# Optimization experiments

Measured on AMD Instinct MI355X. Metric: run time of the kernel, lower is better.

The kernel has to match this reference:

```python
import jax, jax.numpy as jnp
import numpy as np

L = 5   # local window size (l)
R = 2   # upsample factor (r)


def setup_inputs() -> dict:
    key = jax.random.key(0)
    k0, k1, k2 = jax.random.split(key, 3)
    B, C, H, W, OUT = 4, 128, 64, 64, 128
    x = jax.random.normal(k0, (B, C, H, W), jnp.float32)
    # conv1: in_channels -> l^2, 3x3, pad 1 (with bias, as nn.Conv2d default)
    w1 = jax.random.normal(k1, (L * L, C, 3, 3), jnp.float32) * 0.05
    b1 = jnp.zeros((L * L,), jnp.float32)
    # conv2: 4*in_channels -> out_channels, 1x1 (stored as [out, 4C])
    w2 = jax.random.normal(k2, (OUT, 4 * C), jnp.float32) * 0.05
    b2 = jnp.zeros((OUT,), jnp.float32)
    return {"x": x, "w1": w1, "b1": b1, "w2": w2, "b2": b2}


def _upsample2_nearest(t):
    # nearest-neighbor x2 upsample on NCHW
    return jnp.repeat(jnp.repeat(t, R, axis=2), R, axis=3)


def reference(x, w1, b1, w2, b2):
    B, C, H, W = x.shape
    # conv1 (3x3, SAME) -> [B, L^2, H, W]
    k = jax.lax.conv_general_dilated(
        x, w1, window_strides=(1, 1), padding='SAME',
        dimension_numbers=('NCHW', 'OIHW', 'NCHW')) + b1[None, :, None, None]
    # nearest x2 upsample then softmax over the L^2 channel dim
    k = _upsample2_nearest(k)                 # [B, L^2, 2H, 2W]
    k = jax.nn.softmax(k, axis=1)
    # non-overlapping RxR block extraction (unfold size=R, step=R twice)
    # -> [B, L^2, H, W, R^2], last-dim order (row-offset, col-offset)
    k = k.reshape(B, L * L, H, R, W, R).transpose(0, 1, 2, 4, 3, 5)
    k = k.reshape(B, L * L, H, W, R * R)
    # overlapping LxL window extraction of the input (unfold size=L, step=1)
    pad = L // 2
    xp = jnp.pad(x, ((0, 0), (0, 0), (pad, pad), (pad, pad)))
    wins = jnp.stack(
        [xp[:, :, i:i + H, j:j + W] for i in range(L) for j in range(L)],
        axis=-1)                               # [B, C, H, W, L^2]
    # per-pixel matmul: [C, L^2] @ [L^2, R^2] -> [B, H, W, C, R^2]
    out = jnp.einsum('bchwk,bkhwr->bhwcr', wins, k)
    # flatten (C, R^2) -> 4C (C-major, matching torch reshape), back to NCHW
    out = out.reshape(B, H, W, C * R * R).transpose(0, 3, 1, 2)
    out = _upsample2_nearest(out)              # [B, 4C, 2H, 2W]
    # conv2: 1x1 -> out_channels
    out = jnp.einsum('bchw,oc->bohw', out, w2) + b2[None, :, None, None]
    return out
```

## Files before the change

### kernel.cpp

```cpp
#include <hip/hip_runtime.h>
#include <math.h>

#define BB   4
#define CC   128
#define HH   64
#define WW   64
#define OUTC 128
#define KK   25
#define PXB  16
#define SJ   20

typedef __attribute__((ext_vector_type(8))) short short8;
typedef __attribute__((ext_vector_type(4))) float floatx4;

__device__ __forceinline__ unsigned short f32_to_bf16(float v) {
    unsigned int u = __float_as_uint(v);
    u += 0x7fffu + ((u >> 16) & 1u);
    return (unsigned short)(u >> 16);
}
__device__ __forceinline__ float bf16_to_f32(unsigned short h) {
    return __uint_as_float(((unsigned int)h) << 16);
}

__global__ void prep_kernel(const float* __restrict__ w2,
                            const float* __restrict__ w1,
                            unsigned short* __restrict__ w2o,
                            unsigned short* __restrict__ w1f) {
    int i = blockIdx.x * 256 + threadIdx.x;
    if (i < 16384) {
        int o = i >> 7, c = i & 127;
        const float* p = w2 + o * (4 * CC) + c * 4;
        w2o[o * CC + c] = f32_to_bf16(p[0] + p[1] + p[2] + p[3]);
    } else {
        int f = i - 16384;
        int i8 = f & 7;  int rest = f >> 3;
        int lane = rest & 63; rest >>= 6;
        int ks = rest & 3;  rest >>= 2;
        int mt = rest & 1;  rest >>= 1;
        int dydx = rest % 9;
        int wt   = rest / 9;
        int kk = mt * 16 + (lane & 15);
        int c  = ks * 32 + (lane >> 4) * 8 + i8;
        unsigned short o16 = 0;
        if (kk < KK) {
            float v = w1[(size_t)(kk * CC + c) * 9 + dydx];
            unsigned short hi = f32_to_bf16(v);
            o16 = wt ? f32_to_bf16(v - bf16_to_f32(hi)) : hi;
        }
        w1f[f] = o16;
    }
}

__global__ __launch_bounds__(128, 2) void fused_kernel(
        const float* __restrict__ x,
        const unsigned short* __restrict__ w1f,
        const unsigned short* __restrict__ w2o,
        const float* __restrict__ b1,
        const float* __restrict__ b2,
        float* __restrict__ out) {
    __shared__ unsigned short xs_hi[3 * SJ * 128];
    __shared__ unsigned short xs_lo[3 * SJ * 128];
    __shared__ float pk[KK * PXB];
    __shared__ float blds[32];
    unsigned short* sKT = xs_hi;

    int bid0 = blockIdx.x;
    int bid  = (bid0 & 7) * 128 + (bid0 >> 3);
    int wq = bid & 3;
    int h  = (bid >> 2) & 63;
    int b  = bid >> 8;
    int t  = threadIdx.x;
    int lane = t & 63;
    int wv = t >> 6;

    const float* xb = x + (size_t)b * CC * (HH * WW);

    if (t < KK) blds[t] = b1[t];
    {
        int jj = lane & 15, cc = lane >> 4;
        int j  = jj + 2;
        int swz = (j & 15) << 3;
        for (int ci = 0; ci < 16; ++ci) {
            int c  = wv * 64 + ci * 4 + cc;
            int cs = c ^ swz;
            const float* xc = xb + (size_t)c * (HH * WW) + wq * 16 + jj;
            #pragma unroll
            for (int r = 0; r < 3; ++r) {
                int y = h - 1 + r;
                float v = (y >= 0 && y < HH) ? xc[y * WW] : 0.f;
                unsigned short hi = f32_to_bf16(v);
                unsigned short lo = f32_to_bf16(v - bf16_to_f32(hi));
                xs_hi[(r * SJ + j) * 128 + cs] = hi;
                xs_lo[(r * SJ + j) * 128 + cs] = lo;
            }
        }
        for (int i = t; i < 3 * 4 * 128; i += 128) {
            int jh = i & 3;
            int c  = (i >> 2) & 127;
            int r  = i >> 9;
            int j2 = (jh < 2) ? jh : 16 + jh;
            int xcol = wq * 16 + j2 - 2;
            int y = h - 1 + r;
            float v = (xcol >= 0 && xcol < WW && y >= 0 && y < HH)
                    ? xb[(size_t)c * (HH * WW) + y * WW + xcol] : 0.f;
            unsigned short hi = f32_to_bf16(v);
            unsigned short lo = f32_to_bf16(v - bf16_to_f32(hi));
            int cs2 = c ^ ((j2 & 15) << 3);
            xs_hi[(r * SJ + j2) * 128 + cs2] = hi;
            xs_lo[(r * SJ + j2) * 128 + cs2] = lo;
        }
    }
    __syncthreads();

    int fpx = lane & 15, quad = lane >> 4;
    int mt = wv;
    floatx4 acc = {0.f, 0.f, 0.f, 0.f};
    for (int dydx = 0; dydx < 9; ++dydx) {
        int r   = dydx / 3;
        int dxm = dydx - 3 * r;
        int j   = fpx + dxm + 1;
        int rowbase = (r * SJ + j) * 128;
        int swz = (j & 15) << 3;
        const unsigned short* whb = w1f + (dydx * 2 + mt) * 2048 + lane * 8;
        #pragma unroll
        for (int ks = 0; ks < 4; ++ks) {
            int cb = (ks * 32 + quad * 8) ^ swz;
            short8 Ah = *(const short8*)(whb + ks * 512);
            short8 Al = *(const short8*)(whb + 36864 + ks * 512);
            short8 Bh = *(const short8*)&xs_hi[rowbase + cb];
            short8 Bl = *(const short8*)&xs_lo[rowbase + cb];
            acc = __builtin_amdgcn_mfma_f32_16x16x32_bf16(Ah, Bh, acc, 0, 0, 0);
            acc = __builtin_amdgcn_mfma_f32_16x16x32_bf16(Ah, Bl, acc, 0, 0, 0);
            acc = __builtin_amdgcn_mfma_f32_16x16x32_bf16(Al, Bh, acc, 0, 0, 0);
        }
    }
    #pragma unroll
    for (int reg = 0; reg < 4; ++reg) {
        int kk = mt * 16 + quad * 4 + reg;
        if (kk < KK) pk[kk * PXB + fpx] = acc[reg] + blds[kk];
    }
    __syncthreads();

    int pp2 = t & 7, cw = t >> 3;

    float2 lg[KK];
    #pragma unroll
    for (int k = 0; k < KK; ++k) lg[k] = *(const float2*)&pk[k * PXB + 2 * pp2];
    float m0 = -1e30f, m1 = -1e30f;
    #pragma unroll
    for (int k = 0; k < KK; ++k) { m0 = fmaxf(m0, lg[k].x); m1 = fmaxf(m1, lg[k].y); }
    float s0 = 0.f, s1 = 0.f;
    #pragma unroll
    for (int k = 0; k < KK; ++k) {
        lg[k].x = __expf(lg[k].x - m0); s0 += lg[k].x;
        lg[k].y = __expf(lg[k].y - m1); s1 += lg[k].y;
    }
    float i0 = 1.f / s0, i1 = 1.f / s1;
    #pragma unroll
    for (int k = 0; k < KK; ++k) { lg[k].x *= i0; lg[k].y *= i1; }

    int colg = wq * 16 + 2 * pp2 - 2;
    int coff[3]; float cmask[3];
    #pragma unroll
    for (int jx = 0; jx < 3; ++jx) {
        int cg = colg + 2 * jx;
        cmask[jx] = (cg >= 0 && cg <= WW - 2) ? 1.f : 0.f;
        coff[jx]  = min(max(cg, 0), WW - 2);
    }
    int yoff[5]; float msk[15];
    #pragma unroll
    for (int di = 0; di < 5; ++di) {
        int y = h + di - 2;
        float rm = (y >= 0 && y < HH) ? 1.f : 0.f;
        yoff[di] = min(max(y, 0), HH - 1) * WW;
        #pragma unroll
        for (int jx = 0; jx < 3; ++jx) msk[di * 3 + jx] = rm * cmask[jx];
    }

    #pragma unroll 2
    for (int i8 = 0; i8 < 8; ++i8) {
        int c = i8 * 16 + cw;
        const float* xc = xb + (size_t)c * (HH * WW);
        float2 xv[15];
        #pragma unroll
        for (int di = 0; di < 5; ++di)
            #pragma unroll
            for (int jx = 0; jx < 3; ++jx) {
                float2 v = *(const float2*)(xc + yoff[di] + coff[jx]);
                float mm = msk[di * 3 + jx];
                xv[di * 3 + jx] = make_float2(v.x * mm, v.y * mm);
            }
        float t0 = 0.f, t1 = 0.f;
        #pragma unroll
        for (int di = 0; di < 5; ++di) {
            float2 x01 = xv[di * 3 + 0];
            float2 x23 = xv[di * 3 + 1];
            float2 x45 = xv[di * 3 + 2];
            t0 += lg[di*5+0].x * x01.x + lg[di*5+1].x * x01.y
                + lg[di*5+2].x * x23.x + lg[di*5+3].x * x23.y
                + lg[di*5+4].x * x45.x;
            t1 += lg[di*5+0].y * x01.y + lg[di*5+1].y * x23.x
                + lg[di*5+2].y * x23.y + lg[di*5+3].y * x45.x
                + lg[di*5+4].y * x45.y;
        }
        sKT[(2 * pp2) * 136 + c]     = f32_to_bf16(t0);
        sKT[(2 * pp2 + 1) * 136 + c] = f32_to_bf16(t1);
    }
    __syncthreads();

    floatx4 am[4] = {{0.f,0.f,0.f,0.f},{0.f,0.f,0.f,0.f},
                     {0.f,0.f,0.f,0.f},{0.f,0.f,0.f,0.f}};
    #pragma unroll
    for (int ks = 0; ks < 4; ++ks) {
        short8 bf = *(const short8*)&sKT[fpx * 136 + ks*32 + quad*8];
        #pragma unroll
        for (int mt2 = 0; mt2 < 4; ++mt2) {
            short8 af = *(const short8*)&w2o[(size_t)(64*wv + 16*mt2 + fpx) * CC
                                             + ks*32 + quad*8];
            am[mt2] = __builtin_amdgcn_mfma_f32_16x16x32_bf16(af, bf, am[mt2], 0, 0, 0);
        }
    }

    float* ob = out + (size_t)b * OUTC * (4 * HH * WW);
    int y0 = 2 * h;
    int pxo = wq * 16 + fpx;
    #pragma unroll
    for (int mt2 = 0; mt2 < 4; ++mt2) {
        #pragma unroll
        for (int reg = 0; reg < 4; ++reg) {
            int o = 64*wv + 16*mt2 + quad*4 + reg;
            float v = am[mt2][reg] + b2[o];
            float2 v2 = make_float2(v, v);
            float* r0p = ob + ((size_t)o * (2*HH) + y0) * (2*WW) + 2*pxo;
            *(float2*)(r0p)        = v2;
            *(float2*)(r0p + 2*WW) = v2;
        }
    }
}

extern "C" void kernel_launch(void* const* d_in, const int* in_sizes, int n_in,
                              void* d_out, int out_size, void* d_ws, size_t ws_size,
                              hipStream_t stream) {
    const float* x  = (const float*)d_in[0];
    const float* w1 = (const float*)d_in[1];
    const float* b1 = (const float*)d_in[2];
    const float* w2 = (const float*)d_in[3];
    const float* b2 = (const float*)d_in[4];
    float* out = (float*)d_out;

    unsigned short* w2o = (unsigned short*)d_ws;
    unsigned short* w1f = w2o + (size_t)OUTC * CC;

    prep_kernel<<<(16384 + 73728) / 256, 256, 0, stream>>>(w2, w1, w2o, w1f);
    fused_kernel<<<BB * HH * 4, 128, 0, stream>>>(x, w1f, w2o, b1, b2, out);
}
```

Baseline: 104.8 us.

## Replace split-bf16 conv1 MFMA with single fp16 MFMA and prefetch window loads

Conv1 no longer uses a three-MFMA hi/lo bf16 split to emulate higher precision. It now converts weights and input to fp16 and issues one f16 MFMA per k-step, which cuts MFMA count, halves the staging shared memory, and shrinks the prep kernel. The local-window gather loop becomes explicitly double-buffered so global loads for the next channel group overlap the current compute. The bias LDS buffer is dropped and read directly. fp16 has less exponent range and fewer mantissa bits than the split-bf16 scheme, which risks accuracy in the softmax logits.

```diff
diff --git a/kernel.cpp b/kernel.cpp
--- a/kernel.cpp
+++ b/kernel.cpp
@@ -11,15 +11,14 @@
 #define SJ   20
 
 typedef __attribute__((ext_vector_type(8))) short short8;
+typedef _Float16 half8  __attribute__((ext_vector_type(8)));
+typedef __fp16   fp16x2 __attribute__((ext_vector_type(2)));
 typedef __attribute__((ext_vector_type(4))) float floatx4;
 
 __device__ __forceinline__ unsigned short f32_to_bf16(float v) {
     unsigned int u = __float_as_uint(v);
     u += 0x7fffu + ((u >> 16) & 1u);
     return (unsigned short)(u >> 16);
-}
-__device__ __forceinline__ float bf16_to_f32(unsigned short h) {
-    return __uint_as_float(((unsigned int)h) << 16);
 }
 
 __global__ void prep_kernel(const float* __restrict__ w2,
@@ -31,23 +30,18 @@
         int o = i >> 7, c = i & 127;
         const float* p = w2 + o * (4 * CC) + c * 4;
         w2o[o * CC + c] = f32_to_bf16(p[0] + p[1] + p[2] + p[3]);
-    } else {
+    } else if (i < 16384 + 36864) {
         int f = i - 16384;
-        int i8 = f & 7;  int rest = f >> 3;
-        int lane = rest & 63; rest >>= 6;
-        int ks = rest & 3;  rest >>= 2;
-        int mt = rest & 1;  rest >>= 1;
-        int dydx = rest % 9;
-        int wt   = rest / 9;
+        int i8   = f & 7;
+        int lane = (f >> 3) & 63;
+        int ks   = (f >> 9) & 3;
+        int mt   = (f >> 11) & 1;
+        int dydx = f >> 12;
         int kk = mt * 16 + (lane & 15);
         int c  = ks * 32 + (lane >> 4) * 8 + i8;
-        unsigned short o16 = 0;
-        if (kk < KK) {
-            float v = w1[(size_t)(kk * CC + c) * 9 + dydx];
-            unsigned short hi = f32_to_bf16(v);
-            o16 = wt ? f32_to_bf16(v - bf16_to_f32(hi)) : hi;
-        }
-        w1f[f] = o16;
+        float v = (kk < KK) ? w1[(size_t)(kk * CC + c) * 9 + dydx] : 0.f;
+        _Float16 hv = (_Float16)v;
+        w1f[f] = *(unsigned short*)&hv;
     }
 }
 
@@ -58,11 +52,9 @@
         const float* __restrict__ b1,
         const float* __restrict__ b2,
         float* __restrict__ out) {
-    __shared__ unsigned short xs_hi[3 * SJ * 128];
-    __shared__ unsigned short xs_lo[3 * SJ * 128];
+    __shared__ _Float16 xs[3 * SJ * 128];
     __shared__ float pk[KK * PXB];
-    __shared__ float blds[32];
-    unsigned short* sKT = xs_hi;
+    unsigned short* sKT = (unsigned short*)xs;
 
     int bid0 = blockIdx.x;
     int bid  = (bid0 & 7) * 128 + (bid0 >> 3);
@@ -75,23 +67,23 @@
 
     const float* xb = x + (size_t)b * CC * (HH * WW);
 
-    if (t < KK) blds[t] = b1[t];
     {
-        int jj = lane & 15, cc = lane >> 4;
+        int jj = lane & 15, cp = lane >> 4;
         int j  = jj + 2;
         int swz = (j & 15) << 3;
-        for (int ci = 0; ci < 16; ++ci) {
-            int c  = wv * 64 + ci * 4 + cc;
+        #pragma unroll
+        for (int ci = 0; ci < 8; ++ci) {
+            int c  = wv * 64 + ci * 8 + cp * 2;
             int cs = c ^ swz;
-            const float* xc = xb + (size_t)c * (HH * WW) + wq * 16 + jj;
+            const float* xc0 = xb + (size_t)c * (HH * WW) + wq * 16 + jj;
+            const float* xc1 = xc0 + HH * WW;
             #pragma unroll
             for (int r = 0; r < 3; ++r) {
                 int y = h - 1 + r;
-                float v = (y >= 0 && y < HH) ? xc[y * WW] : 0.f;
-                unsigned short hi = f32_to_bf16(v);
-                unsigned short lo = f32_to_bf16(v - bf16_to_f32(hi));
-                xs_hi[(r * SJ + j) * 128 + cs] = hi;
-                xs_lo[(r * SJ + j) * 128 + cs] = lo;
+                float v0 = 0.f, v1 = 0.f;
+                if (y >= 0 && y < HH) { v0 = xc0[y * WW]; v1 = xc1[y * WW]; }
+                fp16x2 p = __builtin_amdgcn_cvt_pkrtz(v0, v1);
+                *(fp16x2*)&xs[(r * SJ + j) * 128 + cs] = p;
             }
         }
         for (int i = t; i < 3 * 4 * 128; i += 128) {
@@ -103,11 +95,7 @@
             int y = h - 1 + r;
             float v = (xcol >= 0 && xcol < WW && y >= 0 && y < HH)
                     ? xb[(size_t)c * (HH * WW) + y * WW + xcol] : 0.f;
-            unsigned short hi = f32_to_bf16(v);
-            unsigned short lo = f32_to_bf16(v - bf16_to_f32(hi));
-            int cs2 = c ^ ((j2 & 15) << 3);
-            xs_hi[(r * SJ + j2) * 128 + cs2] = hi;
-            xs_lo[(r * SJ + j2) * 128 + cs2] = lo;
+            xs[(r * SJ + j2) * 128 + (c ^ ((j2 & 15) << 3))] = (_Float16)v;
         }
     }
     __syncthreads();
@@ -115,6 +103,7 @@
     int fpx = lane & 15, quad = lane >> 4;
     int mt = wv;
     floatx4 acc = {0.f, 0.f, 0.f, 0.f};
+    #pragma unroll
     for (int dydx = 0; dydx < 9; ++dydx) {
         int r   = dydx / 3;
         int dxm = dydx - 3 * r;
@@ -125,19 +114,15 @@
         #pragma unroll
         for (int ks = 0; ks < 4; ++ks) {
             int cb = (ks * 32 + quad * 8) ^ swz;
-            short8 Ah = *(const short8*)(whb + ks * 512);
-            short8 Al = *(const short8*)(whb + 36864 + ks * 512);
-            short8 Bh = *(const short8*)&xs_hi[rowbase + cb];
-            short8 Bl = *(const short8*)&xs_lo[rowbase + cb];
-            acc = __builtin_amdgcn_mfma_f32_16x16x32_bf16(Ah, Bh, acc, 0, 0, 0);
-            acc = __builtin_amdgcn_mfma_f32_16x16x32_bf16(Ah, Bl, acc, 0, 0, 0);
-            acc = __builtin_amdgcn_mfma_f32_16x16x32_bf16(Al, Bh, acc, 0, 0, 0);
+            half8 A = *(const half8*)(whb + ks * 512);
+            half8 B = *(const half8*)&xs[rowbase + cb];
+            acc = __builtin_amdgcn_mfma_f32_16x16x32_f16(A, B, acc, 0, 0, 0);
         }
     }
     #pragma unroll
     for (int reg = 0; reg < 4; ++reg) {
         int kk = mt * 16 + quad * 4 + reg;
-        if (kk < KK) pk[kk * PXB + fpx] = acc[reg] + blds[kk];
+        if (kk < KK) pk[kk * PXB + fpx] = acc[reg] + b1[kk];
     }
     __syncthreads();
 
@@ -177,34 +162,47 @@
         for (int jx = 0; jx < 3; ++jx) msk[di * 3 + jx] = rm * cmask[jx];
     }
 
-    #pragma unroll 2
-    for (int i8 = 0; i8 < 8; ++i8) {
-        int c = i8 * 16 + cw;
-        const float* xc = xb + (size_t)c * (HH * WW);
-        float2 xv[15];
-        #pragma unroll
-        for (int di = 0; di < 5; ++di)
-            #pragma unroll
-            for (int jx = 0; jx < 3; ++jx) {
-                float2 v = *(const float2*)(xc + yoff[di] + coff[jx]);
-                float mm = msk[di * 3 + jx];
-                xv[di * 3 + jx] = make_float2(v.x * mm, v.y * mm);
-            }
-        float t0 = 0.f, t1 = 0.f;
-        #pragma unroll
-        for (int di = 0; di < 5; ++di) {
-            float2 x01 = xv[di * 3 + 0];
-            float2 x23 = xv[di * 3 + 1];
-            float2 x45 = xv[di * 3 + 2];
-            t0 += lg[di*5+0].x * x01.x + lg[di*5+1].x * x01.y
-                + lg[di*5+2].x * x23.x + lg[di*5+3].x * x23.y
-                + lg[di*5+4].x * x45.x;
-            t1 += lg[di*5+0].y * x01.y + lg[di*5+1].y * x23.x
-                + lg[di*5+2].y * x23.y + lg[di*5+3].y * x45.x
-                + lg[di*5+4].y * x45.y;
-        }
-        sKT[(2 * pp2) * 136 + c]     = f32_to_bf16(t0);
-        sKT[(2 * pp2 + 1) * 136 + c] = f32_to_bf16(t1);
+#define LOADC(BUF, I8) do {                                            \
+    int c_ = (I8) * 16 + cw;                                           \
+    const float* xc_ = xb + (size_t)c_ * (HH * WW);                    \
+    _Pragma("unroll")                                                  \
+    for (int di = 0; di < 5; ++di)                                     \
+        _Pragma("unroll")                                              \
+        for (int jx = 0; jx < 3; ++jx)                                 \
+            BUF[di * 3 + jx] = *(const float2*)(xc_ + yoff[di] + coff[jx]); \
+} while (0)
+
+#define COMPST(BUF, I8) do {                                           \
+    float t0 = 0.f, t1 = 0.f;                                          \
+    _Pragma("unroll")                                                  \
+    for (int di = 0; di < 5; ++di) {                                   \
+        float2 x01 = BUF[di * 3 + 0];                                  \
+        float2 x23 = BUF[di * 3 + 1];                                  \
+        float2 x45 = BUF[di * 3 + 2];                                  \
+        x01.x *= msk[di * 3 + 0]; x01.y *= msk[di * 3 + 0];            \
+        x23.x *= msk[di * 3 + 1]; x23.y *= msk[di * 3 + 1];            \
+        x45.x *= msk[di * 3 + 2]; x45.y *= msk[di * 3 + 2];            \
+        t0 += lg[di*5+0].x * x01.x + lg[di*5+1].x * x01.y              \
+            + lg[di*5+2].x * x23.x + lg[di*5+3].x * x23.y              \
+            + lg[di*5+4].x * x45.x;                                    \
+        t1 += lg[di*5+0].y * x01.y + lg[di*5+1].y * x23.x              \
+            + lg[di*5+2].y * x23.y + lg[di*5+3].y * x45.x              \
+            + lg[di*5+4].y * x45.y;                                    \
+    }                                                                  \
+    int cs_ = (I8) * 16 + cw;                                          \
+    sKT[(2 * pp2) * 136 + cs_]     = f32_to_bf16(t0);                  \
+    sKT[(2 * pp2 + 1) * 136 + cs_] = f32_to_bf16(t1);                  \
+} while (0)
+
+    {
+        float2 bufA[15], bufB[15];
+        LOADC(bufA, 0);
+        for (int it = 0; it < 4; ++it) {
+            LOADC(bufB, 2 * it + 1);
+            COMPST(bufA, 2 * it);
+            if (it < 3) LOADC(bufA, 2 * it + 2);
+            COMPST(bufB, 2 * it + 1);
+        }
     }
     __syncthreads();
 
@@ -251,6 +249,6 @@
     unsigned short* w2o = (unsigned short*)d_ws;
     unsigned short* w1f = w2o + (size_t)OUTC * CC;
 
-    prep_kernel<<<(16384 + 73728) / 256, 256, 0, stream>>>(w2, w1, w2o, w1f);
+    prep_kernel<<<(16384 + 36864 + 255) / 256, 256, 0, stream>>>(w2, w1, w2o, w1f);
     fused_kernel<<<BB * HH * 4, 128, 0, stream>>>(x, w1f, w2o, b1, b2, out);
 }
```

Measured after the change: 94.94 us. -9.4%, faster.
